# Performance work log

Measured on AMD Instinct MI355X. Metric: run time of the kernel, lower is better.

The kernel has to match this reference:

```python
import jax, jax.numpy as jnp
import numpy as np
from jax import lax

T_MAX, BATCH, CLASSES, L_MAX = 512, 32, 1296, 64
NINF = -jnp.inf


def _align_one(logsm, label, C, R):
    """Monotonic max-probability forced alignment for one sample.
    logsm: [T, V] log-probs, label: [L] int, C=x_len (valid frames), R=label_len.
    Returns per-frame pseudo target [T] (0-padded past C)."""
    T, V = logsm.shape
    L = label.shape[0]
    rows = jnp.arange(L)
    cols = jnp.arange(T)
    # pb[i, j] = logsm[j, label[i]], restricted to the monotonic band i <= j <= C-R+i
    pb = logsm[:, label].T  # [L, T]
    band = (cols[None, :] >= rows[:, None]) & (cols[None, :] <= C - R + rows[:, None]) & (rows[:, None] < R)
    pb = jnp.where(band, pb, NINF)

    # Forward DP over time columns: dp[i,j] = max(dp[i-1,j-1], dp[i,j-1]) + pb[i,j]
    # (strict > for the diagonal move, exactly as the original numpy code).
    dp0 = jnp.where(rows == 0, pb[:, 0], NINF)

    def step(dp, pb_col):
        shifted = jnp.concatenate([jnp.full((1,), NINF, dp.dtype), dp[:-1]])
        choice = shifted > dp  # True -> came from (i-1, j-1)
        dp_new = jnp.where(choice, shifted, dp) + pb_col
        return dp_new, choice

    _, choices = lax.scan(step, dp0, pb.T[1:])  # [T-1, L] bool
    choices = jnp.concatenate([jnp.zeros((1, L), bool), choices], axis=0)  # [T, L]

    # Backtrack from (R-1, C-1); columns j >= C emit padding 0.
    def bstep(row, jc):
        j, ch = jc
        active = j < C
        tgt = jnp.where(active, label[row], 0)
        row_new = jnp.where(active, row - ch[row].astype(row.dtype), row)
        return row_new, tgt

    row0 = (R - 1).astype(jnp.int32)
    _, targets = lax.scan(bstep, row0, (jnp.arange(T), choices), reverse=True)
    return targets  # [T]


def _make_targets(logsm, label, x_len, label_len):
    # logsm: [T, B, V] -> targets [T, B]
    return jax.vmap(_align_one, in_axes=(1, 0, 0, 0))(logsm, label, x_len, label_len).T


def setup_inputs() -> dict:
    key = jax.random.key(0)
    k0, k1, k2, k3, k4 = jax.random.split(key, 5)
    pred = jax.random.normal(k0, (T_MAX, BATCH, CLASSES), jnp.float32)
    seq_pred = jax.random.normal(k1, (T_MAX, BATCH, CLASSES), jnp.float32)
    label = jax.random.randint(k2, (BATCH, L_MAX), 0, CLASSES)
    x_len = jax.random.randint(k3, (BATCH,), T_MAX // 2, T_MAX + 1)  # >= L_MAX so band is valid
    label_len = jax.random.randint(k4, (BATCH,), 8, L_MAX + 1)
    return {"pred": pred, "seq_pred": seq_pred, "label": label, "x_len": x_len, "label_len": label_len}


def reference(pred, seq_pred, label, x_len, label_len):
    T, B, V = pred.shape
    logsm_seq = jax.nn.log_softmax(seq_pred, axis=-1)
    target = _make_targets(logsm_seq, label, x_len, label_len)  # [T, B] int
    probs = jnp.exp(logsm_seq)  # softmax(seq_pred)
    conf = jnp.take_along_axis(probs, target[..., None], axis=2)[..., 0]  # [T, B]
    smooth = (1.0 - conf) / (V - 1)
    onehot = jax.nn.one_hot(target, V, dtype=pred.dtype)  # [T, B, V]
    true_dist = jnp.where(onehot > 0, conf[..., None], smooth[..., None])
    mask = (jnp.arange(T)[:, None] < x_len[None, :]).astype(pred.dtype)  # [T, B]
    ce = jnp.sum(-true_dist * jax.nn.log_softmax(pred, axis=-1), axis=-1) * mask
    return jnp.mean(ce)
```

## Files before the change

### kernel.cpp

```cpp
#include <hip/hip_runtime.h>

#define T_MAX 512
#define BATCH 32
#define CLASSES 1296
#define L_MAX 64
#define NROWS (T_MAX * BATCH)
#define NINF (-INFINITY)
#define COLSTRIDE (BATCH * CLASSES)

__device__ __forceinline__ float wave_sum64(float v) {
    v += __int_as_float(__builtin_amdgcn_update_dpp(0, __float_as_int(v), 0x111, 0xF, 0xF, true));
    v += __int_as_float(__builtin_amdgcn_update_dpp(0, __float_as_int(v), 0x112, 0xF, 0xF, true));
    v += __int_as_float(__builtin_amdgcn_update_dpp(0, __float_as_int(v), 0x114, 0xF, 0xF, true));
    v += __int_as_float(__builtin_amdgcn_update_dpp(0, __float_as_int(v), 0x118, 0xF, 0xF, true));
    v += __int_as_float(__builtin_amdgcn_update_dpp(0, __float_as_int(v), 0x142, 0xF, 0xF, true));
    v += __int_as_float(__builtin_amdgcn_update_dpp(0, __float_as_int(v), 0x143, 0xF, 0xF, true));
    return v;
}

__global__ __launch_bounds__(256) void mega_kernel(
    const float* __restrict__ pred, const float* __restrict__ seqp,
    const int* __restrict__ label, const int* __restrict__ x_len,
    const int* __restrict__ label_len,
    float* __restrict__ lse_pred, float* __restrict__ sum_pred,
    float* __restrict__ lse_seq, int* __restrict__ tg,
    int* __restrict__ counter)
{
    __shared__ unsigned chw[1024];
    __shared__ int a_s[64];
    __shared__ int rows_s[T_MAX];

    if (blockIdx.x < 32) {
        if (threadIdx.x >= 64) return;
        const int b = blockIdx.x, lane = threadIdx.x;
        if (b == 0 && lane == 0) *counter = 0;
        const int C = x_len[b], R = label_len[b];
        const int limit = C - R;
        const int lab = label[(b << 6) + lane];
        const float* gsrc = seqp + (size_t)b * CLASSES + lab;
        const int P = (C + 31) >> 5;
        const float biasR = (lane < R) ? 0.f : NINF;
        const bool isb0 = (lane & 15) == 0;
        const int ninf_i = 0xFF800000;

        float va[32], vb[32];
        float dp = NINF;

#define LOAD_PANEL(VV, LDP) {                                                  \
        const float* s_ = gsrc + (size_t)(LDP) * 32 * COLSTRIDE;               \
        _Pragma("unroll")                                                      \
        for (int u = 0; u < 32; ++u) VV[u] = s_[(size_t)u * COLSTRIDE];        \
    }

#define COMPUTE_PANEL(VV, PP) {                                                \
        const int base = (PP) << 5;                                            \
        unsigned w0 = 0;                                                       \
        _Pragma("unroll")                                                      \
        for (int g = 0; g < 2; ++g) {                                          \
            const bool general = ((PP) == 0) || (base + (g << 4) + 15 > limit);\
            _Pragma("unroll")                                                  \
            for (int u = 0; u < 16; ++u) {                                     \
                const int kk = (g << 4) + u;                                   \
                const int j = base + kk;                                       \
                float val;                                                     \
                if (general) {                                                 \
                    if ((PP) == 0 && kk == 0) {             \
                        dp = (lane == 0) ? VV[0] : NINF;                       \
                        continue;                                              \
                    }                                                          \
                    const bool ib = (lane <= j) && (lane >= j - limit) && (lane < R); \
                    val = ib ? VV[kk] : NINF;                                  \
                } else {                                                       \
                    val = VV[kk] + biasR;                  \
                }                                                              \
                const int dpb = __float_as_int(dp);                            \
                const int t1 = __builtin_amdgcn_update_dpp(ninf_i, dpb, 0x111, 0xF, 0xF, false);  \
                const int t2 = __builtin_amdgcn_update_dpp(ninf_i, dpb, 0x142, 0xF, 0xF, false);  \
                const float shifted = __int_as_float(isb0 ? t2 : t1);          \
                const bool c = shifted > dp;               \
                w0 |= (c ? 1u : 0u) << kk;                                     \
                dp = fmaxf(shifted, dp) + val;             \
            }                                                                  \
        }                                                                      \
        chw[((PP) << 6) + lane] = w0;                                          \
    }

        LOAD_PANEL(va, 0)
        for (int p = 0; p < P; p += 2) {
            int l1 = p + 1; if (l1 >= P) l1 = P - 1;
            LOAD_PANEL(vb, l1)
            COMPUTE_PANEL(va, p)
            if (p + 1 >= P) break;
            int l2 = p + 2; if (l2 >= P) l2 = P - 1;
            LOAD_PANEL(va, l2)
            COMPUTE_PANEL(vb, p + 1)
        }
#undef LOAD_PANEL
#undef COMPUTE_PANEL

        if (lane == 0) {
            int row = R - 1, j = C - 1;
            while (row > 0 && j >= 0) {
                unsigned word = chw[((j >> 5) << 6) + row];
                unsigned mb = (2u << (j & 31)) - 1;
                unsigned m = word & mb;
                if (m) {
                    int hb = 31 - __clz(m);
                    int aj = (j & ~31) | hb;
                    a_s[row] = aj;
                    row--; j = aj - 1;
                } else {
                    j = (j & ~31) - 1;
                }
            }
            for (int i = row; i >= 0; --i) a_s[i] = 0;
        }
        if (lane < R) {
            int a = a_s[lane];
            int bi = (lane == R - 1) ? (C - 1) : (a_s[lane + 1] - 1);
            for (int j = a; j <= bi; ++j) rows_s[j] = lane;
        }
        for (int j = lane; j < T_MAX; j += 64)
            tg[(b << 9) + j] = (j < C) ? rows_s[j] : -1;
    } else if (blockIdx.x < 32 + NROWS / 4) {
        int r = (blockIdx.x - 32) * 4 + (threadIdx.x >> 6);
        int lane = threadIdx.x & 63;
        const float* xs = seqp + (size_t)r * CLASSES;
        const float4* s4 = (const float4*)xs;

        float4 b0 = s4[lane],       b1 = s4[lane + 64],  b2 = s4[lane + 128];
        float4 b3 = s4[lane + 192], b4 = s4[lane + 256];
        float4 bt = make_float4(0.f, 0.f, 0.f, 0.f);
        if (lane < 4) bt = s4[320 + lane];

        float ss = __expf(b0.x) + __expf(b0.y) + __expf(b0.z) + __expf(b0.w)
                 + __expf(b1.x) + __expf(b1.y) + __expf(b1.z) + __expf(b1.w)
                 + __expf(b2.x) + __expf(b2.y) + __expf(b2.z) + __expf(b2.w)
                 + __expf(b3.x) + __expf(b3.y) + __expf(b3.z) + __expf(b3.w)
                 + __expf(b4.x) + __expf(b4.y) + __expf(b4.z) + __expf(b4.w);
        if (lane < 4)
            ss += __expf(bt.x) + __expf(bt.y) + __expf(bt.z) + __expf(bt.w);
        ss = wave_sum64(ss);
        if (lane == 63) lse_seq[r] = __logf(ss);
    } else {
        int r = (blockIdx.x - (32 + NROWS / 4)) * 4 + (threadIdx.x >> 6);
        int lane = threadIdx.x & 63;
        const float* xp = pred + (size_t)r * CLASSES;
        const float4* p4 = (const float4*)xp;

        float4 a0 = p4[lane],       a1 = p4[lane + 64],  a2 = p4[lane + 128];
        float4 a3 = p4[lane + 192], a4 = p4[lane + 256];
        float4 at = make_float4(0.f, 0.f, 0.f, 0.f);
        if (lane < 4) at = p4[320 + lane];

        float sp = __expf(a0.x) + __expf(a0.y) + __expf(a0.z) + __expf(a0.w)
                 + __expf(a1.x) + __expf(a1.y) + __expf(a1.z) + __expf(a1.w)
                 + __expf(a2.x) + __expf(a2.y) + __expf(a2.z) + __expf(a2.w)
                 + __expf(a3.x) + __expf(a3.y) + __expf(a3.z) + __expf(a3.w)
                 + __expf(a4.x) + __expf(a4.y) + __expf(a4.z) + __expf(a4.w);
        float sx = (a0.x + a0.y + a0.z + a0.w) + (a1.x + a1.y + a1.z + a1.w)
                 + (a2.x + a2.y + a2.z + a2.w) + (a3.x + a3.y + a3.z + a3.w)
                 + (a4.x + a4.y + a4.z + a4.w);
        if (lane < 4) {
            sp += __expf(at.x) + __expf(at.y) + __expf(at.z) + __expf(at.w);
            sx += at.x + at.y + at.z + at.w;
        }
        sp = wave_sum64(sp);
        sx = wave_sum64(sx);
        if (lane == 63) {
            lse_pred[r] = __logf(sp);
            sum_pred[r] = sx;
        }
    }
}

__global__ __launch_bounds__(256) void ce_kernel(
    const float* __restrict__ pred, const float* __restrict__ seqp,
    const int* __restrict__ label, const int* __restrict__ x_len,
    const float* __restrict__ lse_pred, const float* __restrict__ sum_pred,
    const float* __restrict__ lse_seq,
    const int* __restrict__ tg, float* __restrict__ partials,
    int* __restrict__ counter, float* __restrict__ out)
{
    int e = blockIdx.x * 256 + threadIdx.x;
    int t = e >> 5, b = e & 31;
    float ce = 0.f;
    if (t < x_len[b]) {
        int row = tg[(b << 9) + t];
        int tgt = label[(b << 6) + row];
        float lp = lse_pred[e];
        float S = sum_pred[e] - (float)CLASSES * lp;
        float lsp_t = pred[(size_t)e * CLASSES + tgt] - lp;
        float conf = __expf(seqp[(size_t)e * CLASSES + tgt] - lse_seq[e]);
        float smooth = (1.f - conf) * (1.f / (float)(CLASSES - 1));
        ce = -((conf - smooth) * lsp_t + smooth * S);
    }
    ce = wave_sum64(ce);
    __shared__ float sm[4];
    __shared__ int amLast;
    if ((threadIdx.x & 63) == 63) sm[threadIdx.x >> 6] = ce;
    __syncthreads();
    if (threadIdx.x == 0) {
        float p = sm[0] + sm[1] + sm[2] + sm[3];
        __hip_atomic_store(&partials[blockIdx.x], p, __ATOMIC_RELEASE, __HIP_MEMORY_SCOPE_AGENT);
        amLast = (__hip_atomic_fetch_add(counter, 1, __ATOMIC_ACQ_REL, __HIP_MEMORY_SCOPE_AGENT) == 63);
    }
    __syncthreads();
    if (amLast && threadIdx.x < 64) {
        float v = __hip_atomic_load(&partials[threadIdx.x], __ATOMIC_ACQUIRE, __HIP_MEMORY_SCOPE_AGENT);
        for (int o = 32; o; o >>= 1) v += __shfl_down(v, o, 64);
        if (threadIdx.x == 0) out[0] = v * (1.0f / (float)NROWS);
    }
}

extern "C" void kernel_launch(void* const* d_in, const int* in_sizes, int n_in,
                              void* d_out, int out_size, void* d_ws, size_t ws_size,
                              hipStream_t stream) {
    const float* pred      = (const float*)d_in[0];
    const float* seq_pred  = (const float*)d_in[1];
    const int*   label     = (const int*)d_in[2];
    const int*   x_len     = (const int*)d_in[3];
    const int*   label_len = (const int*)d_in[4];
    float* out = (float*)d_out;

    float* w = (float*)d_ws;
    float* lse_pred = w;
    float* sum_pred = w + NROWS;
    float* lse_seq  = w + 2 * NROWS;
    int*   tg       = (int*)(w + 3 * NROWS);
    float* partials = (float*)(tg + NROWS);
    int*   counter  = (int*)(partials + 64);

    mega_kernel<<<32 + NROWS / 2, 256, 0, stream>>>(pred, seq_pred, label,
                                                    x_len, label_len,
                                                    lse_pred, sum_pred, lse_seq,
                                                    tg, counter);
    ce_kernel<<<64, 256, 0, stream>>>(pred, seq_pred, label, x_len,
                                      lse_pred, sum_pred, lse_seq, tg,
                                      partials, counter, out);
}
```

Measured before the change: 215.1 us.

## Stage DP gather panels through LDS double buffer to cut register pressure

Replaces the two 32-float register panels in the alignment DP with a single register gather buffer plus a double-buffered shared-memory staging area. Each panel is gathered from global memory, written to LDS, and read back 16 values at a time during the serial DP, so the next gather overlaps the current compute. It also adds a min-blocks-per-CU hint of 4 to the launch bounds. The aim is fewer VGPRs and better occupancy, at the cost of extra LDS traffic and 16KB more shared memory per block, which also applies to the other blocks that share this kernel.

```diff
diff --git a/kernel.cpp b/kernel.cpp
--- a/kernel.cpp
+++ b/kernel.cpp
@@ -18,7 +18,7 @@
     return v;
 }
 
-__global__ __launch_bounds__(256) void mega_kernel(
+__global__ __launch_bounds__(256, 4) void mega_kernel(
     const float* __restrict__ pred, const float* __restrict__ seqp,
     const int* __restrict__ label, const int* __restrict__ x_len,
     const int* __restrict__ label_len,
@@ -26,6 +26,7 @@
     float* __restrict__ lse_seq, int* __restrict__ tg,
     int* __restrict__ counter)
 {
+    __shared__ float abuf[2][2048];
     __shared__ unsigned chw[1024];
     __shared__ int a_s[64];
     __shared__ int rows_s[T_MAX];
@@ -43,35 +44,45 @@
         const bool isb0 = (lane & 15) == 0;
         const int ninf_i = 0xFF800000;
 
-        float va[32], vb[32];
+        float g[32];
         float dp = NINF;
 
-#define LOAD_PANEL(VV, LDP) {                                                  \
+#define GATHER(LDP) {                                                          \
         const float* s_ = gsrc + (size_t)(LDP) * 32 * COLSTRIDE;               \
         _Pragma("unroll")                                                      \
-        for (int u = 0; u < 32; ++u) VV[u] = s_[(size_t)u * COLSTRIDE];        \
-    }
-
-#define COMPUTE_PANEL(VV, PP) {                                                \
+        for (int u = 0; u < 32; ++u) g[u] = s_[(size_t)u * COLSTRIDE];         \
+    }
+
+#define WRITE_PANEL(BUF) {                                                     \
+        float* d_ = abuf[BUF];                                                 \
+        _Pragma("unroll")                                                      \
+        for (int u = 0; u < 32; ++u) d_[(u << 6) + lane] = g[u];               \
+    }
+
+#define COMPUTE_PANEL(BUF, PP) {                                               \
+        const float* bc = abuf[BUF];                                           \
         const int base = (PP) << 5;                                            \
         unsigned w0 = 0;                                                       \
         _Pragma("unroll")                                                      \
-        for (int g = 0; g < 2; ++g) {                                          \
-            const bool general = ((PP) == 0) || (base + (g << 4) + 15 > limit);\
+        for (int gg = 0; gg < 2; ++gg) {                                       \
+            float v[16];                                                       \
+            _Pragma("unroll")                                                  \
+            for (int u = 0; u < 16; ++u) v[u] = bc[(((gg << 4) + u) << 6) + lane]; \
+            const bool general = ((PP) == 0) || (base + (gg << 4) + 15 > limit); \
             _Pragma("unroll")                                                  \
             for (int u = 0; u < 16; ++u) {                                     \
-                const int kk = (g << 4) + u;                                   \
+                const int kk = (gg << 4) + u;                                  \
                 const int j = base + kk;                                       \
                 float val;                                                     \
                 if (general) {                                                 \
                     if ((PP) == 0 && kk == 0) {             \
-                        dp = (lane == 0) ? VV[0] : NINF;                       \
+                        dp = (lane == 0) ? v[0] : NINF;                        \
                         continue;                                              \
                     }                                                          \
                     const bool ib = (lane <= j) && (lane >= j - limit) && (lane < R); \
-                    val = ib ? VV[kk] : NINF;                                  \
+                    val = ib ? v[u] : NINF;                                    \
                 } else {                                                       \
-                    val = VV[kk] + biasR;                  \
+                    val = v[u] + biasR;                    \
                 }                                                              \
                 const int dpb = __float_as_int(dp);                            \
                 const int t1 = __builtin_amdgcn_update_dpp(ninf_i, dpb, 0x111, 0xF, 0xF, false);  \
@@ -85,17 +96,17 @@
         chw[((PP) << 6) + lane] = w0;                                          \
     }
 
-        LOAD_PANEL(va, 0)
-        for (int p = 0; p < P; p += 2) {
-            int l1 = p + 1; if (l1 >= P) l1 = P - 1;
-            LOAD_PANEL(vb, l1)
-            COMPUTE_PANEL(va, p)
-            if (p + 1 >= P) break;
-            int l2 = p + 2; if (l2 >= P) l2 = P - 1;
-            LOAD_PANEL(va, l2)
-            COMPUTE_PANEL(vb, p + 1)
-        }
-#undef LOAD_PANEL
+        GATHER(0)
+        WRITE_PANEL(0)
+        GATHER(1)
+        for (int p = 0; p < P; ++p) {
+            COMPUTE_PANEL(p & 1, p)
+            WRITE_PANEL((p + 1) & 1)
+            int nl = p + 2; if (nl >= P) nl = P - 1;
+            GATHER(nl)
+        }
+#undef GATHER
+#undef WRITE_PANEL
 #undef COMPUTE_PANEL
 
         if (lane == 0) {
```

New measurement: 220.5 us. 2.5% more time.

## Stream gathered label probabilities from seq blocks to alignment waves via flag counters

Applied to the files above, without the earlier changes.

The seq log-softmax blocks now stage each row in shared memory, gather the 64 label-indexed probabilities, and publish them to a compact per-batch buffer. Each publish bumps a per-panel counter with release semantics. Alignment is packed into 4 blocks of 8 waves, and each wave spin-waits on those counters before reading contiguous coalesced panels. This replaces the strided uncoalesced gathers from the full seq tensor and overlaps alignment with the row reductions. It relies on the producer blocks being scheduled while the consumers spin, which risks deadlock or stalls, and it adds a memset plus larger blocks with a shared-memory union.

```diff
diff --git a/kernel.cpp b/kernel.cpp
--- a/kernel.cpp
+++ b/kernel.cpp
@@ -6,7 +6,10 @@
 #define L_MAX 64
 #define NROWS (T_MAX * BATCH)
 #define NINF (-INFINITY)
-#define COLSTRIDE (BATCH * CLASSES)
+
+#define ALIGNBLK 4
+#define NSEQBLK 2048
+#define NPREDBLK 2048
 
 __device__ __forceinline__ float wave_sum64(float v) {
     v += __int_as_float(__builtin_amdgcn_update_dpp(0, __float_as_int(v), 0x111, 0xF, 0xF, true));
@@ -18,113 +21,125 @@
     return v;
 }
 
-__global__ __launch_bounds__(256) void mega_kernel(
+struct AlignSh {
+    unsigned chw[8][1024];
+    int a_s[8][64];
+    int rows_s[8][T_MAX];
+};
+union ShU {
+    AlignSh al;
+    float rowbuf[8][CLASSES];
+};
+
+__global__ __launch_bounds__(512, 3) void mega_kernel(
     const float* __restrict__ pred, const float* __restrict__ seqp,
     const int* __restrict__ label, const int* __restrict__ x_len,
     const int* __restrict__ label_len,
     float* __restrict__ lse_pred, float* __restrict__ sum_pred,
-    float* __restrict__ lse_seq, int* __restrict__ tg,
-    int* __restrict__ counter)
+    float* __restrict__ lse_seq, float* __restrict__ pb,
+    int* __restrict__ tg, int* __restrict__ cnt, int* __restrict__ counter)
 {
-    __shared__ unsigned chw[1024];
-    __shared__ int a_s[64];
-    __shared__ int rows_s[T_MAX];
-
-    if (blockIdx.x < 32) {
-        if (threadIdx.x >= 64) return;
-        const int b = blockIdx.x, lane = threadIdx.x;
-        if (b == 0 && lane == 0) *counter = 0;
+    __shared__ ShU sh;
+    const int w = threadIdx.x >> 6, lane = threadIdx.x & 63;
+
+    if (blockIdx.x < ALIGNBLK) {
+        if (blockIdx.x == 0 && threadIdx.x == 0) *counter = 0;
+        const int b = (blockIdx.x << 3) + w;
         const int C = x_len[b], R = label_len[b];
         const int limit = C - R;
-        const int lab = label[(b << 6) + lane];
-        const float* gsrc = seqp + (size_t)b * CLASSES + lab;
+        const float* pbb = pb + ((size_t)b << 15);
+        int* cntb = cnt + (b << 4);
         const int P = (C + 31) >> 5;
         const float biasR = (lane < R) ? 0.f : NINF;
         const bool isb0 = (lane & 15) == 0;
         const int ninf_i = 0xFF800000;
-
-        float va[32], vb[32];
+        unsigned* chwl = sh.al.chw[w];
+
+        float va[16], vb[16];
         float dp = NINF;
-
-#define LOAD_PANEL(VV, LDP) {                                                  \
-        const float* s_ = gsrc + (size_t)(LDP) * 32 * COLSTRIDE;               \
+        unsigned w0 = 0;
+
+#define WAITP(PP) while (__hip_atomic_load(&cntb[PP], __ATOMIC_ACQUIRE,        \
+                          __HIP_MEMORY_SCOPE_AGENT) < 32)                      \
+                      __builtin_amdgcn_s_sleep(2);
+
+#define GLOAD(VV, GG) {                                                        \
+        const float* s_ = pbb + ((GG) << 10);                                  \
         _Pragma("unroll")                                                      \
-        for (int u = 0; u < 32; ++u) VV[u] = s_[(size_t)u * COLSTRIDE];        \
-    }
-
-#define COMPUTE_PANEL(VV, PP) {                                                \
-        const int base = (PP) << 5;                                            \
-        unsigned w0 = 0;                                                       \
+        for (int u = 0; u < 16; ++u)                                           \
+            VV[u] = __hip_atomic_load(&s_[(u << 6) + lane], __ATOMIC_RELAXED,  \
+                                      __HIP_MEMORY_SCOPE_AGENT);               \
+    }
+
+#define COMPUTE16(VV, GG) {                                                    \
+        const int g_ = (GG);                                                   \
+        const bool general = (g_ < 2) || (((g_ << 4) + 15) > limit);           \
         _Pragma("unroll")                                                      \
-        for (int g = 0; g < 2; ++g) {                                          \
-            const bool general = ((PP) == 0) || (base + (g << 4) + 15 > limit);\
-            _Pragma("unroll")                                                  \
-            for (int u = 0; u < 16; ++u) {                                     \
-                const int kk = (g << 4) + u;                                   \
-                const int j = base + kk;                                       \
-                float val;                                                     \
-                if (general) {                                                 \
-                    if ((PP) == 0 && kk == 0) {             \
-                        dp = (lane == 0) ? VV[0] : NINF;                       \
-                        continue;                                              \
-                    }                                                          \
-                    const bool ib = (lane <= j) && (lane >= j - limit) && (lane < R); \
-                    val = ib ? VV[kk] : NINF;                                  \
-                } else {                                                       \
-                    val = VV[kk] + biasR;                  \
+        for (int u = 0; u < 16; ++u) {                                         \
+            const int j = (g_ << 4) + u;                                       \
+            float val;                                                         \
+            if (general) {                                                     \
+                if (g_ == 0 && u == 0) {                    \
+                    dp = (lane == 0) ? VV[0] : NINF;                           \
+                    continue;                                                  \
                 }                                                              \
-                const int dpb = __float_as_int(dp);                            \
-                const int t1 = __builtin_amdgcn_update_dpp(ninf_i, dpb, 0x111, 0xF, 0xF, false);  \
-                const int t2 = __builtin_amdgcn_update_dpp(ninf_i, dpb, 0x142, 0xF, 0xF, false);  \
-                const float shifted = __int_as_float(isb0 ? t2 : t1);          \
-                const bool c = shifted > dp;               \
-                w0 |= (c ? 1u : 0u) << kk;                                     \
-                dp = fmaxf(shifted, dp) + val;             \
+                const bool ib = (lane <= j) && (lane >= j - limit) && (lane < R); \
+                val = ib ? VV[u] : NINF;                                       \
+            } else {                                                           \
+                val = VV[u] + biasR;                     \
             }                                                                  \
+            const int dpb = __float_as_int(dp);                                \
+            const int t1 = __builtin_amdgcn_update_dpp(ninf_i, dpb, 0x111, 0xF, 0xF, false);  \
+            const int t2 = __builtin_amdgcn_update_dpp(ninf_i, dpb, 0x142, 0xF, 0xF, false);  \
+            const float shifted = __int_as_float(isb0 ? t2 : t1);              \
+            const bool c = shifted > dp;                \
+            w0 |= (c ? 1u : 0u) << (j & 31);                                   \
+            dp = fmaxf(shifted, dp) + val;            \
         }                                                                      \
-        chw[((PP) << 6) + lane] = w0;                                          \
-    }
-
-        LOAD_PANEL(va, 0)
-        for (int p = 0; p < P; p += 2) {
-            int l1 = p + 1; if (l1 >= P) l1 = P - 1;
-            LOAD_PANEL(vb, l1)
-            COMPUTE_PANEL(va, p)
-            if (p + 1 >= P) break;
-            int l2 = p + 2; if (l2 >= P) l2 = P - 1;
-            LOAD_PANEL(va, l2)
-            COMPUTE_PANEL(vb, p + 1)
-        }
-#undef LOAD_PANEL
-#undef COMPUTE_PANEL
+    }
+
+        WAITP(0)
+        GLOAD(va, 0)
+        for (int p = 0; p < P; ++p) {
+            const int g0 = p << 1;
+            GLOAD(vb, g0 + 1)
+            w0 = 0;
+            COMPUTE16(va, g0)
+            if (p + 1 < P) { WAITP(p + 1) GLOAD(va, g0 + 2) }
+            COMPUTE16(vb, g0 + 1)
+            chwl[(p << 6) + lane] = w0;
+        }
+#undef WAITP
+#undef GLOAD
+#undef COMPUTE16
 
         if (lane == 0) {
             int row = R - 1, j = C - 1;
             while (row > 0 && j >= 0) {
-                unsigned word = chw[((j >> 5) << 6) + row];
+                unsigned word = chwl[((j >> 5) << 6) + row];
                 unsigned mb = (2u << (j & 31)) - 1;
                 unsigned m = word & mb;
                 if (m) {
                     int hb = 31 - __clz(m);
                     int aj = (j & ~31) | hb;
-                    a_s[row] = aj;
+                    sh.al.a_s[w][row] = aj;
                     row--; j = aj - 1;
                 } else {
                     j = (j & ~31) - 1;
                 }
             }
-            for (int i = row; i >= 0; --i) a_s[i] = 0;
+            for (int i = row; i >= 0; --i) sh.al.a_s[w][i] = 0;
         }
         if (lane < R) {
-            int a = a_s[lane];
-            int bi = (lane == R - 1) ? (C - 1) : (a_s[lane + 1] - 1);
-            for (int j = a; j <= bi; ++j) rows_s[j] = lane;
+            int a = sh.al.a_s[w][lane];
+            int bi = (lane == R - 1) ? (C - 1) : (sh.al.a_s[w][lane + 1] - 1);
+            for (int j = a; j <= bi; ++j) sh.al.rows_s[w][j] = lane;
         }
         for (int j = lane; j < T_MAX; j += 64)
-            tg[(b << 9) + j] = (j < C) ? rows_s[j] : -1;
-    } else if (blockIdx.x < 32 + NROWS / 4) {
-        int r = (blockIdx.x - 32) * 4 + (threadIdx.x >> 6);
-        int lane = threadIdx.x & 63;
+            tg[(b << 9) + j] = (j < C) ? sh.al.rows_s[w][j] : -1;
+    } else if (blockIdx.x < ALIGNBLK + NSEQBLK) {
+        const int r = ((blockIdx.x - ALIGNBLK) << 3) + w;
+        const int t = r >> 5, b = r & 31;
         const float* xs = seqp + (size_t)r * CLASSES;
         const float4* s4 = (const float4*)xs;
 
@@ -132,6 +147,12 @@
         float4 b3 = s4[lane + 192], b4 = s4[lane + 256];
         float4 bt = make_float4(0.f, 0.f, 0.f, 0.f);
         if (lane < 4) bt = s4[320 + lane];
+        const int lab = label[(b << 6) + lane];
+
+        float4* rb4 = (float4*)sh.rowbuf[w];
+        rb4[lane] = b0; rb4[lane + 64] = b1; rb4[lane + 128] = b2;
+        rb4[lane + 192] = b3; rb4[lane + 256] = b4;
+        if (lane < 4) rb4[320 + lane] = bt;
 
         float ss = __expf(b0.x) + __expf(b0.y) + __expf(b0.z) + __expf(b0.w)
                  + __expf(b1.x) + __expf(b1.y) + __expf(b1.z) + __expf(b1.w)
@@ -142,9 +163,15 @@
             ss += __expf(bt.x) + __expf(bt.y) + __expf(bt.z) + __expf(bt.w);
         ss = wave_sum64(ss);
         if (lane == 63) lse_seq[r] = __logf(ss);
+
+        float pbv = sh.rowbuf[w][lab];
+        __hip_atomic_store(&pb[(((size_t)(b << 9) + t) << 6) + lane], pbv,
+                           __ATOMIC_RELAXED, __HIP_MEMORY_SCOPE_AGENT);
+        if (lane == 0)
+            __hip_atomic_fetch_add(&cnt[(b << 4) + (t >> 5)], 1,
+                                   __ATOMIC_RELEASE, __HIP_MEMORY_SCOPE_AGENT);
     } else {
-        int r = (blockIdx.x - (32 + NROWS / 4)) * 4 + (threadIdx.x >> 6);
-        int lane = threadIdx.x & 63;
+        const int r = ((blockIdx.x - (ALIGNBLK + NSEQBLK)) << 3) + w;
         const float* xp = pred + (size_t)r * CLASSES;
         const float4* p4 = (const float4*)xp;
 
@@ -223,18 +250,20 @@
     const int*   label_len = (const int*)d_in[4];
     float* out = (float*)d_out;
 
-    float* w = (float*)d_ws;
-    float* lse_pred = w;
-    float* sum_pred = w + NROWS;
-    float* lse_seq  = w + 2 * NROWS;
-    int*   tg       = (int*)(w + 3 * NROWS);
+    float* ws = (float*)d_ws;
+    float* lse_pred = ws;
+    float* sum_pred = ws + NROWS;
+    float* lse_seq  = ws + 2 * NROWS;
+    float* pb       = ws + 3 * NROWS;
+    int*   tg       = (int*)(pb + (size_t)BATCH * T_MAX * 64);
     float* partials = (float*)(tg + NROWS);
     int*   counter  = (int*)(partials + 64);
-
-    mega_kernel<<<32 + NROWS / 2, 256, 0, stream>>>(pred, seq_pred, label,
-                                                    x_len, label_len,
-                                                    lse_pred, sum_pred, lse_seq,
-                                                    tg, counter);
+    int*   cnt      = counter + 1;
+
+    hipMemsetAsync(cnt, 0, 512 * sizeof(int), stream);
+    mega_kernel<<<ALIGNBLK + NSEQBLK + NPREDBLK, 512, 0, stream>>>(
+        pred, seq_pred, label, x_len, label_len,
+        lse_pred, sum_pred, lse_seq, pb, tg, cnt, counter);
     ce_kernel<<<64, 256, 0, stream>>>(pred, seq_pred, label, x_len,
                                       lse_pred, sum_pred, lse_seq, tg,
                                       partials, counter, out);
```

Result: slower. 635.7 us (+195.5%).
